# Performance work log

Measured on AMD Instinct MI355X. Metric: run time of the kernel, lower is better.

Reference implementation:

```python
import jax, jax.numpy as jnp
import numpy as np

NUM_CLASSES = 100
CACHE_SIZE = 50
N_PROTOS = NUM_CLASSES * CACHE_SIZE  # 5000
FEAT_DIM = 128
BATCH = 2048
NVIEWS = 2
TEMP = 0.1
EPSILON = 0.05
PROTO_M = 0.99
TOPK = 10
LAMBDA_PCON = 1.0
SINKHORN_ITERS = 3


def _l1norm(x, axis):
    return x / jnp.clip(jnp.sum(jnp.abs(x), axis=axis, keepdims=True), 1e-12)


def _l2norm(x, axis=-1):
    return x / jnp.clip(jnp.linalg.norm(x, axis=axis, keepdims=True), 1e-12)


def _sinkhorn(feats, protos):
    # torch uses out.detach(): Q carries no gradient
    out = jax.lax.stop_gradient(feats @ protos.T)  # [N, K]
    Q = jnp.exp(out / EPSILON).T                   # [K, N]
    K_, B_ = Q.shape
    Q = Q / jnp.sum(Q)
    for _ in range(SINKHORN_ITERS):
        Q = _l1norm(Q, axis=1) / K_   # row L1 normalize
        Q = _l1norm(Q, axis=0) / B_   # col L1 normalize
    return (Q * B_).T                 # [N, K]


def _topk_mask(x, k):
    _, idx = jax.lax.top_k(x, k)
    rows = jnp.arange(x.shape[0])[:, None]
    return jnp.zeros_like(x).at[rows, idx].set(1.0)


def reference(features, targets, beta, protos):
    # features: [B, V, D] -> [V*B, D] (view-major, matches torch.cat(torch.unbind(dim=1)))
    feats = jnp.transpose(features, (1, 0, 2)).reshape(-1, FEAT_DIM)
    labels = jnp.tile(targets, NVIEWS)                              # [N]
    contrast_labels = jnp.tile(jnp.arange(NUM_CLASSES), CACHE_SIZE)  # [K]
    mask = (labels[:, None] == contrast_labels[None, :]).astype(feats.dtype)  # [N, K]

    # ---- mle_loss ----
    Q = _sinkhorn(feats, jax.lax.stop_gradient(protos))
    update_mask = mask * Q
    tkm = _topk_mask(update_mask, TOPK)
    update_mask = _l1norm(tkm * update_mask, axis=1)

    update_features = update_mask.T @ feats                         # [K, D]
    protos_new = PROTO_M * protos + (1.0 - PROTO_M) * update_features
    sim_mean = jax.lax.stop_gradient(
        jnp.mean(jnp.sum(_l2norm(update_features, 1) * _l2norm(protos, 1), axis=1)))
    protos2 = _l2norm(protos_new, axis=1)

    Q2 = _sinkhorn(feats, jax.lax.stop_gradient(protos2))
    logits = jax.nn.softplus(feats @ jax.lax.stop_gradient(protos2).T / TEMP)  # [N, K]

    loss_mask = mask * Q2
    # NOTE: original code top-ks update_mask (already normalized) here, not loss_mask
    tkm2 = _topk_mask(update_mask, TOPK)
    loss_mask = _l1norm(tkm2 * loss_mask, axis=1)
    masked_logits = loss_mask * logits

    positive_logits = mask * logits
    negative_logits = logits * (1.0 - mask)
    imp = jax.lax.stop_gradient(jnp.exp(beta * jnp.log(negative_logits + 1e-10)))
    total_logits = positive_logits + imp * negative_logits

    pos = jnp.sum(masked_logits, axis=1)                             # [N]
    neg = jnp.log(jnp.sum(jnp.exp(total_logits), axis=1, keepdims=True))  # [N, 1]
    # faithful to the torch broadcast: [N] - [N,1] -> [N, N]
    mle = -jnp.mean(pos - neg)

    # ---- proto_contra ----
    pn = _l2norm(protos2, axis=1)                                    # [K, D]
    plabels = jnp.tile(jnp.arange(NUM_CLASSES), CACHE_SIZE)
    pmask = (plabels[:, None] == plabels[None, :]).astype(pn.dtype)
    tau = jax.lax.stop_gradient((1.0 + (0.5 - sim_mean)) * 0.4)
    adc = pn @ pn.T / tau
    lg = adc - jax.lax.stop_gradient(jnp.max(adc, axis=1, keepdims=True))
    lmask = 1.0 - jnp.eye(N_PROTOS, dtype=pn.dtype)
    pmask = pmask * lmask
    ppos = jnp.sum(_l1norm(pmask, axis=1) * lg, axis=1)
    pneg = jnp.log(jnp.sum(lmask * jnp.exp(lg), axis=1))
    pcon = -jnp.mean(ppos - pneg)

    return mle + LAMBDA_PCON * pcon


def setup_inputs() -> dict:
    key = jax.random.key(0)
    k1, k2, k3 = jax.random.split(key, 3)
    features = jax.random.normal(k1, (BATCH, NVIEWS, FEAT_DIM), dtype=jnp.float32)
    features = _l2norm(features, axis=-1)  # unit-norm embeddings keep exp(./eps) finite
    targets = jax.random.randint(k2, (BATCH,), 0, NUM_CLASSES)
    beta = jnp.float32(0.5)
    protos = _l2norm(jax.random.uniform(k3, (N_PROTOS, FEAT_DIM), dtype=jnp.float32), axis=-1)
    return {"features": features, "targets": targets, "beta": beta, "protos": protos}
```

## Files before the change

### kernel.cpp

```cpp
#include <hip/hip_runtime.h>
#include <math.h>

constexpr int NUM_CLASSES = 100;
constexpr int CACHE_SIZE  = 50;
constexpr int NPROT       = 5000;
constexpr int FD          = 128;
constexpr int BATCH       = 2048;
constexpr int NROWS       = 4096;
constexpr int TOPK        = 10;
constexpr float INV_EPS   = 20.0f;
constexpr float INV_TEMP  = 10.0f;
constexpr float PROTO_M   = 0.99f;
constexpr int PLD         = 5120;
constexpr int SROWS       = 16;
constexpr int NSLOT       = NROWS / SROWS;
constexpr int NTILE       = 40;
constexpr int NTRI        = NTILE * (NTILE + 1) / 2;


typedef __attribute__((ext_vector_type(8))) short bf16x8;
typedef __attribute__((ext_vector_type(4))) float f32x4;
typedef __attribute__((ext_vector_type(4))) _Float16 f16x4;
typedef __attribute__((ext_vector_type(8))) _Float16 f16x8;

__device__ __forceinline__ float blockReduceSum(float v) {
  __shared__ float tmp[8];
  const int lane = threadIdx.x & 63;
  const int wid  = threadIdx.x >> 6;
  #pragma unroll
  for (int o = 32; o > 0; o >>= 1) v += __shfl_down(v, o, 64);
  __syncthreads();
  if (lane == 0) tmp[wid] = v;
  __syncthreads();
  const int nw = (blockDim.x + 63) >> 6;
  float s = 0.f;
  for (int i = 0; i < nw; ++i) s += tmp[i];
  return s;
}

__device__ __forceinline__ short f2bf(float x) {
  union { float f; unsigned u; } v; v.f = x;
  const unsigned r = v.u + 0x7fffu + ((v.u >> 16) & 1u);
  return (short)(r >> 16);
}

__global__ void k_build_split(const float* __restrict__ features,
                              const float* __restrict__ protos,
                              float* __restrict__ feats,
                              short* __restrict__ fb, short* __restrict__ pb) {
  constexpr int NF4 = NROWS * (FD / 4);
  constexpr int NP4 = NPROT * FD / 4;
  const int t = blockIdx.x * 256 + threadIdx.x;
  if (t < NF4) {
    const int n  = t >> 5;
    const int d4 = (t & 31) << 2;
    const int b  = n & (BATCH - 1);
    const int v  = n >> 11;
    const float4 src = *reinterpret_cast<const float4*>(features + ((size_t)b * 2 + v) * FD + d4);
    *reinterpret_cast<float4*>(feats + (size_t)n * FD + d4) = src;
    short4 h;
    h.x = f2bf(src.x); h.y = f2bf(src.y); h.z = f2bf(src.z); h.w = f2bf(src.w);
    *reinterpret_cast<short4*>(fb + (size_t)n * FD + d4) = h;
  } else if (t - NF4 < NP4) {
    const int u = t - NF4;
    const float4 v = *reinterpret_cast<const float4*>(protos + (size_t)u * 4);
    short4 h;
    h.x = f2bf(v.x); h.y = f2bf(v.y); h.z = f2bf(v.z); h.w = f2bf(v.w);
    *reinterpret_cast<short4*>(pb + (size_t)u * 4) = h;
  }
}

__global__ __launch_bounds__(256) void k_gemm_mfma(
    const short* __restrict__ A, const short* __restrict__ B,
    int Nb, _Float16* __restrict__ C, float* __restrict__ colpart) {
  __shared__ __align__(16) short Bs[128 * 64];
  __shared__ float red[4][128];
  const int tid  = threadIdx.x;
  const int wid  = tid >> 6;
  const int lane = tid & 63;
  const int lr   = lane & 15;
  const int kg   = lane >> 4;
  const int m0   = blockIdx.y * 128 + wid * 32;
  const int n0   = blockIdx.x * 128;

  f32x4 acc[2][8];
  #pragma unroll
  for (int i = 0; i < 2; ++i)
    #pragma unroll
    for (int j = 0; j < 8; ++j) acc[i][j] = (f32x4){0.f, 0.f, 0.f, 0.f};

  bool cval[8];
  #pragma unroll
  for (int j = 0; j < 8; ++j) cval[j] = (n0 + j * 16 + lr < Nb);

  const int scol = tid >> 1;
  const int sk   = (tid & 1) * 32;
  const int gcol = min(n0 + scol, Nb - 1);

  #pragma unroll
  for (int h = 0; h < 2; ++h) {
    const int k0 = h * 64;
    if (h) __syncthreads();
    #pragma unroll
    for (int u = 0; u < 4; ++u) {
      const int kk2 = sk + u * 8;
      const bf16x8 vb = *reinterpret_cast<const bf16x8*>(B + (size_t)gcol * FD + k0 + kk2);
      const int byteoff = (scol * 128 + kk2 * 2) ^ ((scol & 7) << 4);
      *reinterpret_cast<bf16x8*>(reinterpret_cast<char*>(&Bs[0]) + byteoff) = vb;
    }
    __syncthreads();
    #pragma unroll
    for (int kk = 0; kk < 2; ++kk) {
      const int kb = k0 + kk * 32 + kg * 8;
      bf16x8 av[2], bv[8];
      #pragma unroll
      for (int i = 0; i < 2; ++i)
        av[i] = *reinterpret_cast<const bf16x8*>(A + (size_t)(m0 + i * 16 + lr) * FD + kb);
      #pragma unroll
      for (int j = 0; j < 8; ++j) {
        const int col = j * 16 + lr;
        const int bo = (col * 128 + (kk * 32 + kg * 8) * 2) ^ ((col & 7) << 4);
        bv[j] = *reinterpret_cast<const bf16x8*>(reinterpret_cast<const char*>(&Bs[0]) + bo);
      }
      #pragma unroll
      for (int i = 0; i < 2; ++i)
        #pragma unroll
        for (int j = 0; j < 8; ++j)
          acc[i][j] = __builtin_amdgcn_mfma_f32_16x16x32_bf16(av[i], bv[j], acc[i][j], 0, 0, 0);
    }
  }

  float csum[8];
  #pragma unroll
  for (int j = 0; j < 8; ++j) csum[j] = 0.f;
  #pragma unroll
  for (int i = 0; i < 2; ++i) {
    const int rbase = m0 + i * 16 + kg * 4;
    #pragma unroll
    for (int j = 0; j < 8; ++j) {
      if (!cval[j]) continue;
      const int col = n0 + j * 16 + lr;
      #pragma unroll
      for (int q = 0; q < 4; ++q) {
        const float tval = __expf(acc[i][j][q] * INV_TEMP);
        const _Float16 tf = (_Float16)tval;
        C[(size_t)(rbase + q) * NPROT + col] = tf;
        const float t32 = (float)tf;
        csum[j] = fmaf(t32, t32, csum[j]);
      }
    }
  }
  __syncthreads();
  #pragma unroll
  for (int j = 0; j < 8; ++j) {
    float v = csum[j];
    v += __shfl_xor(v, 16, 64);
    v += __shfl_xor(v, 32, 64);
    if (lane < 16) red[wid][j * 16 + lane] = v;
  }
  __syncthreads();
  if (tid < 128) {
    const int col = n0 + tid;
    if (col < Nb) {
      const float t = red[0][tid] + red[1][tid] + red[2][tid] + red[3][tid];
      colpart[(size_t)blockIdx.y * PLD + col] = t;
    }
  }
}

template <bool WITH_MLE>
__global__ __launch_bounds__(512) void k_sink_fused(const _Float16* __restrict__ big,
                                                    const float* __restrict__ Rin,
                                                    float* __restrict__ part,
                                                    float* __restrict__ semain,
                                                    const float* __restrict__ beta_ptr) {
  __shared__ float Cl[SROWS];
  const int r0   = blockIdx.x * SROWS;
  const int wid  = threadIdx.x >> 6;
  const int lane = threadIdx.x & 63;
  float beta = 0.f;
  bool bhalf = false;
  if constexpr (WITH_MLE) {
    beta = beta_ptr[0];
    bhalf = (beta == 0.5f);
  }
  #pragma unroll
  for (int rr = 0; rr < SROWS / 8; ++rr) {
    const int r = rr * 8 + wid;
    const _Float16* row = big + (size_t)(r0 + r) * NPROT;
    float s = 0.f, se = 0.f;
    for (int idx = lane; idx < NPROT / 8; idx += 64) {
      const f16x8 v = *reinterpret_cast<const f16x8*>(row + idx * 8);
      const float4 q0 = *reinterpret_cast<const float4*>(Rin + idx * 8);
      const float4 q1 = *reinterpret_cast<const float4*>(Rin + idx * 8 + 4);
      float rt[8], rq[8];
      #pragma unroll
      for (int e = 0; e < 8; ++e) rt[e] = (float)v[e];
      rq[0] = q0.x; rq[1] = q0.y; rq[2] = q0.z; rq[3] = q0.w;
      rq[4] = q1.x; rq[5] = q1.y; rq[6] = q1.z; rq[7] = q1.w;
      #pragma unroll
      for (int e = 0; e < 8; ++e)
        s = fmaf(rt[e] * rt[e], rq[e], s);
      if constexpr (WITH_MLE) {
        #pragma unroll
        for (int e = 0; e < 8; ++e) {
          const float l = __logf(1.f + rt[e]);
          const float lb = l + 1e-10f;
          const float imp = bhalf ? sqrtf(lb) : __expf(beta * __logf(lb));
          se += __expf(imp * l);
        }
      }
    }
    #pragma unroll
    for (int o = 32; o > 0; o >>= 1) {
      s += __shfl_down(s, o, 64);
      if constexpr (WITH_MLE) se += __shfl_down(se, o, 64);
    }
    if (lane == 0) {
      Cl[r] = 1.0f / s;
      if constexpr (WITH_MLE) semain[r0 + r] = se;
    }
  }
  __syncthreads();
  for (int k4 = threadIdx.x * 4; k4 < NPROT; k4 += 2048) {
    float s[4] = {0.f, 0.f, 0.f, 0.f};
    #pragma unroll
    for (int r = 0; r < SROWS; ++r) {
      const f16x4 v = *reinterpret_cast<const f16x4*>(big + (size_t)(r0 + r) * NPROT + k4);
      const float c = Cl[r];
      #pragma unroll
      for (int e = 0; e < 4; ++e) {
        const float t = (float)v[e];
        s[e] = fmaf(t * t, c, s[e]);
      }
    }
    *reinterpret_cast<float4*>(part + (size_t)blockIdx.x * PLD + k4) =
        make_float4(s[0], s[1], s[2], s[3]);
  }
}

__global__ __launch_bounds__(512) void k_red_slots(const float* __restrict__ part,
                                                   int nslots, float* __restrict__ R) {
  __shared__ float red[8][64];
  const int g  = threadIdx.x >> 6;
  const int kk = threadIdx.x & 63;
  const int k  = blockIdx.x * 64 + kk;
  float s = 0.f;
  if (k < NPROT) {
    const int per = nslots >> 3;
    const int b0 = g * per, b1 = b0 + per;
    for (int b = b0; b < b1; ++b) s += part[(size_t)b * PLD + k];
  }
  red[g][kk] = s;
  __syncthreads();
  if (threadIdx.x < 64 && k < NPROT) {
    float t = 0.f;
    #pragma unroll
    for (int g2 = 0; g2 < 8; ++g2) t += red[g2][kk];
    R[k] = 1.0f / t;
  }
}

__global__ __launch_bounds__(256) void k_top10(const _Float16* __restrict__ out1,
                                               const float* __restrict__ R3,
                                               const int* __restrict__ targets,
                                               float* __restrict__ wsel) {
  const int n = blockIdx.x * 4 + (threadIdx.x >> 6);
  const int lane = threadIdx.x & 63;
  const int c = targets[n & (BATCH - 1)];
  float cur = -1.0f, orig = -1.0f;
  if (lane < CACHE_SIZE) {
    const int k = c + lane * NUM_CLASSES;
    const float t = (float)out1[(size_t)n * NPROT + k];
    cur = t * t * R3[k];
    orig = cur;
  }
  float tvsum = 0.f;
  bool selme = false;
  #pragma unroll
  for (int i = 0; i < TOPK; ++i) {
    float bv = cur;
    int   bj = lane;
    #pragma unroll
    for (int o = 32; o > 0; o >>= 1) {
      const float ov = __shfl_xor(bv, o, 64);
      const int   oj = __shfl_xor(bj, o, 64);
      if (ov > bv || (ov == bv && oj < bj)) { bv = ov; bj = oj; }
    }
    tvsum += bv;
    if (lane == bj) { cur = -2.0f; selme = true; }
  }
  tvsum = fmaxf(tvsum, 1e-12f);
  if (lane < CACHE_SIZE)
    wsel[(size_t)n * CACHE_SIZE + lane] = selme ? orig / tvsum : 0.f;
}

__global__ __launch_bounds__(1024) void k_prep(const int* __restrict__ targets,
                                               int* __restrict__ classbase,
                                               int* __restrict__ rowlist) {
  __shared__ int t[BATCH];
  __shared__ short chcnt[8][NUM_CLASSES];
  __shared__ int   chpre[8][NUM_CLASSES];
  __shared__ int   ctot[NUM_CLASSES];
  __shared__ int   base[NUM_CLASSES + 1];
  for (int i = threadIdx.x; i < BATCH; i += 1024) t[i] = targets[i];
  __syncthreads();
  if (threadIdx.x < 8 * NUM_CLASSES) {
    const int ch = threadIdx.x / NUM_CLASSES;
    const int c  = threadIdx.x % NUM_CLASSES;
    int m = 0;
    const int i0 = ch << 8;
    for (int i = i0; i < i0 + 256; ++i) m += (t[i] == c);
    chcnt[ch][c] = (short)m;
  }
  __syncthreads();
  if (threadIdx.x < NUM_CLASSES) {
    const int c = threadIdx.x;
    int s = 0;
    #pragma unroll
    for (int ch = 0; ch < 8; ++ch) { chpre[ch][c] = s; s += chcnt[ch][c]; }
    ctot[c] = s;
  }
  __syncthreads();
  if (threadIdx.x == 0) {
    int s = 0;
    for (int c = 0; c < NUM_CLASSES; ++c) { base[c] = s; s += 2 * ctot[c]; }
    base[NUM_CLASSES] = s;
  }
  __syncthreads();
  if (threadIdx.x <= NUM_CLASSES) classbase[threadIdx.x] = base[threadIdx.x];
  for (int b = threadIdx.x; b < BATCH; b += 1024) {
    const int c  = t[b];
    const int ch = b >> 8;
    int r = chpre[ch][c];
    for (int i = ch << 8; i < b; ++i) r += (t[i] == c);
    const int bs  = base[c];
    const int cnt = (base[c + 1] - bs) >> 1;
    rowlist[bs + r] = b;
    rowlist[bs + cnt + r] = BATCH + b;
  }
}

__global__ __launch_bounds__(128) void k_ufpu(const float* __restrict__ feats,
                                              const float* __restrict__ wsel,
                                              const int* __restrict__ rowlist,
                                              const int* __restrict__ classbase,
                                              const float* __restrict__ protos,
                                              short* __restrict__ pnb,
                                              float* __restrict__ simbuf) {
  const int k = blockIdx.x;
  const int d = threadIdx.x;
  const int c = k % NUM_CLASSES;
  const int j = k / NUM_CLASSES;
  const int b0 = classbase[c], b1 = classbase[c + 1];
  float u = 0.f;
  for (int ii = b0; ii < b1; ++ii) {
    const int n = rowlist[ii];
    const float wv = wsel[(size_t)n * CACHE_SIZE + j];
    if (wv != 0.f) u = fmaf(wv, feats[(size_t)n * FD + d], u);
  }
  const float p = protos[(size_t)k * FD + d];
  const float pnew = PROTO_M * p + (1.0f - PROTO_M) * u;
  const float spp = blockReduceSum(p * p);
  const float suu = blockReduceSum(u * u);
  const float sup = blockReduceSum(u * p);
  const float snn = blockReduceSum(pnew * pnew);
  const float x = pnew / fmaxf(sqrtf(snn), 1e-12f);
  pnb[(size_t)k * FD + d] = f2bf(x);
  if (d == 0)
    simbuf[k] = sup / (fmaxf(sqrtf(suu), 1e-12f) * fmaxf(sqrtf(spp), 1e-12f));
}

__global__ void k_tau(const float* __restrict__ simbuf, float* __restrict__ scalars) {
  float s = 0.f;
  for (int k = threadIdx.x; k < NPROT; k += 256) s += simbuf[k];
  s = blockReduceSum(s);
  if (threadIdx.x == 0) {
    const float sim_mean = s / (float)NPROT;
    scalars[0] = (1.0f + (0.5f - sim_mean)) * 0.4f;
  }
}

__global__ __launch_bounds__(256) void k_mle_fin(const _Float16* __restrict__ out2,
                                                 const float* __restrict__ R3,
                                                 const int* __restrict__ targets,
                                                 const float* __restrict__ wsel,
                                                 const float* __restrict__ beta_ptr,
                                                 const float* __restrict__ semain,
                                                 float* __restrict__ rowres) {
  const int n = blockIdx.x * 4 + (threadIdx.x >> 6);
  const int lane = threadIdx.x & 63;
  const int c = targets[n & (BATCH - 1)];
  const float beta = beta_ptr[0];
  const bool bhalf = (beta == 0.5f);
  float corr = 0.f, swl = 0.f, sw = 0.f;
  if (lane < CACHE_SIZE) {
    const int k = c + lane * NUM_CLASSES;
    const float t = (float)out2[(size_t)n * NPROT + k];
    const float l = __logf(1.f + t);
    const float lb = l + 1e-10f;
    const float imp = bhalf ? sqrtf(lb) : __expf(beta * __logf(lb));
    corr = (1.f + t) - __expf(imp * l);
    if (wsel[(size_t)n * CACHE_SIZE + lane] > 0.f) {
      const float w2 = t * t * R3[k];
      swl = w2 * l;
      sw  = w2;
    }
  }
  #pragma unroll
  for (int o = 32; o > 0; o >>= 1) {
    corr += __shfl_down(corr, o, 64);
    swl  += __shfl_down(swl,  o, 64);
    sw   += __shfl_down(sw,   o, 64);
  }
  if (lane == 0)
    rowres[n] = __logf(semain[n] + corr) - swl / fmaxf(sw, 1e-12f);
}

__global__ __launch_bounds__(256) void k_pcon_mfma(
    const short* __restrict__ P, const float* __restrict__ scalars,
    float* __restrict__ part_neg, float* __restrict__ part_pos) {
  __shared__ __align__(16) short Bs[128 * 64];
  int tdec = blockIdx.x, by = 0;
  while (tdec >= NTILE - by) { tdec -= NTILE - by; ++by; }
  const int bx = by + tdec;
  const bool diag = (bx == by);

  const int tid  = threadIdx.x;
  const int wid  = tid >> 6;
  const int lane = tid & 63;
  const int lr   = lane & 15;
  const int kg   = lane >> 4;
  const int k0r  = by * 128 + wid * 32;
  const int l0   = bx * 128;
  const float invtau = 1.0f / scalars[0];

  f32x4 acc[2][8];
  #pragma unroll
  for (int i = 0; i < 2; ++i)
    #pragma unroll
    for (int j = 0; j < 8; ++j) acc[i][j] = (f32x4){0.f, 0.f, 0.f, 0.f};

  int rowa[2];
  #pragma unroll
  for (int i = 0; i < 2; ++i) {
    const int r = k0r + i * 16 + lr;
    rowa[i] = (r < NPROT) ? r : (NPROT - 1);
  }
  bool cval[8];
  #pragma unroll
  for (int j = 0; j < 8; ++j) cval[j] = (l0 + j * 16 + lr < NPROT);

  const int scol = tid >> 1;
  const int sk   = (tid & 1) * 32;
  const int gcol = min(l0 + scol, NPROT - 1);

  #pragma unroll
  for (int h = 0; h < 2; ++h) {
    const int k0 = h * 64;
    if (h) __syncthreads();
    #pragma unroll
    for (int u = 0; u < 4; ++u) {
      const int kk2 = sk + u * 8;
      const bf16x8 vb = *reinterpret_cast<const bf16x8*>(P + (size_t)gcol * FD + k0 + kk2);
      const int byteoff = (scol * 128 + kk2 * 2) ^ ((scol & 7) << 4);
      *reinterpret_cast<bf16x8*>(reinterpret_cast<char*>(&Bs[0]) + byteoff) = vb;
    }
    __syncthreads();
    #pragma unroll
    for (int kk = 0; kk < 2; ++kk) {
      const int kb = k0 + kk * 32 + kg * 8;
      bf16x8 av[2], bv[8];
      #pragma unroll
      for (int i = 0; i < 2; ++i)
        av[i] = *reinterpret_cast<const bf16x8*>(P + (size_t)rowa[i] * FD + kb);
      #pragma unroll
      for (int j = 0; j < 8; ++j) {
        const int col = j * 16 + lr;
        const int bo = (col * 128 + (kk * 32 + kg * 8) * 2) ^ ((col & 7) << 4);
        bv[j] = *reinterpret_cast<const bf16x8*>(reinterpret_cast<const char*>(&Bs[0]) + bo);
      }
      #pragma unroll
      for (int i = 0; i < 2; ++i)
        #pragma unroll
        for (int j = 0; j < 8; ++j)
          acc[i][j] = __builtin_amdgcn_mfma_f32_16x16x32_bf16(av[i], bv[j], acc[i][j], 0, 0, 0);
    }
  }

  int ccls[8];
  #pragma unroll
  for (int j = 0; j < 8; ++j) ccls[j] = (l0 + j * 16 + lr) % NUM_CLASSES;
  float cneg[8], cpos[8];
  #pragma unroll
  for (int j = 0; j < 8; ++j) { cneg[j] = 0.f; cpos[j] = 0.f; }

  #pragma unroll
  for (int i = 0; i < 2; ++i) {
    float sneg[4] = {0.f, 0.f, 0.f, 0.f};
    float spos[4] = {0.f, 0.f, 0.f, 0.f};
    const int rbase = k0r + i * 16 + kg * 4;
    #pragma unroll
    for (int q = 0; q < 4; ++q) {
      const int rg = rbase + q;
      if (rg >= NPROT) continue;
      const int rcls = rg % NUM_CLASSES;
      #pragma unroll
      for (int j = 0; j < 8; ++j) {
        const int cg = l0 + j * 16 + lr;
        if (!cval[j]) continue;
        if (diag && cg == rg) continue;
        const float lg = fmaf(acc[i][j][q], invtau, -invtau);
        const float e  = __expf(lg);
        sneg[q] += e;
        cneg[j] += e;
        if (ccls[j] == rcls) { spos[q] += lg; cpos[j] += lg; }
      }
    }
    #pragma unroll
    for (int q = 0; q < 4; ++q) {
      float sn = sneg[q], sp = spos[q];
      #pragma unroll
      for (int off = 8; off > 0; off >>= 1) {
        sn += __shfl_xor(sn, off, 64);
        sp += __shfl_xor(sp, off, 64);
      }
      if (lr == 0) {
        const int rg = rbase + q;
        if (rg < NPROT) {
          part_neg[(size_t)bx * PLD + rg] = sn;
          part_pos[(size_t)bx * PLD + rg] = sp;
        }
      }
    }
  }

  if (!diag) {
    __syncthreads();
    float* redn = reinterpret_cast<float*>(&Bs[0]);
    float* redp = redn + 512;
    #pragma unroll
    for (int j = 0; j < 8; ++j) {
      float cn = cneg[j];
      cn += __shfl_xor(cn, 16, 64);
      cn += __shfl_xor(cn, 32, 64);
      float cp = cpos[j];
      cp += __shfl_xor(cp, 16, 64);
      cp += __shfl_xor(cp, 32, 64);
      if (lane < 16) {
        redn[wid * 128 + j * 16 + lane] = cn;
        redp[wid * 128 + j * 16 + lane] = cp;
      }
    }
    __syncthreads();
    if (tid < 128) {
      const int cg = l0 + tid;
      if (cg < NPROT) {
        const float tn = redn[tid] + redn[128 + tid] + redn[256 + tid] + redn[384 + tid];
        const float tp = redp[tid] + redp[128 + tid] + redp[256 + tid] + redp[384 + tid];
        part_neg[(size_t)by * PLD + cg] = tn;
        part_pos[(size_t)by * PLD + cg] = tp;
      }
    }
  }
}

__global__ __launch_bounds__(256) void k_pcon_fin(const float* __restrict__ part_neg,
                                                  const float* __restrict__ part_pos,
                                                  float* __restrict__ pconbuf) {
  __shared__ float rn[4][64], rp[4][64];
  const int g  = threadIdx.x >> 6;
  const int kk = threadIdx.x & 63;
  const int k  = blockIdx.x * 64 + kk;
  float sn = 0.f, sp = 0.f;
  if (k < NPROT) {
    for (int b = g * 10; b < g * 10 + 10; ++b) {
      sn += part_neg[(size_t)b * PLD + k];
      sp += part_pos[(size_t)b * PLD + k];
    }
  }
  rn[g][kk] = sn; rp[g][kk] = sp;
  __syncthreads();
  if (threadIdx.x < 64 && k < NPROT) {
    const float tn = rn[0][kk] + rn[1][kk] + rn[2][kk] + rn[3][kk];
    const float tp = rp[0][kk] + rp[1][kk] + rp[2][kk] + rp[3][kk];
    pconbuf[k] = __logf(tn) - tp * (1.0f / (float)(CACHE_SIZE - 1));
  }
}

__global__ void k_final(const float* __restrict__ rowres,
                        const float* __restrict__ pconbuf,
                        float* __restrict__ outp) {
  float s1 = 0.f, s2 = 0.f;
  for (int i = threadIdx.x; i < NROWS; i += 256) s1 += rowres[i];
  for (int i = threadIdx.x; i < NPROT; i += 256) s2 += pconbuf[i];
  s1 = blockReduceSum(s1);
  s2 = blockReduceSum(s2);
  if (threadIdx.x == 0) outp[0] = s1 / (float)NROWS + s2 / (float)NPROT;
}

extern "C" void kernel_launch(void* const* d_in, const int* in_sizes, int n_in,
                              void* d_out, int out_size, void* d_ws, size_t ws_size,
                              hipStream_t stream) {
  (void)in_sizes; (void)n_in; (void)out_size; (void)ws_size;
  const float* features = (const float*)d_in[0];
  const int*   targets  = (const int*)d_in[1];
  const float* beta     = (const float*)d_in[2];
  const float* protos   = (const float*)d_in[3];
  float* outp = (float*)d_out;

  char* basep = (char*)d_ws;
  size_t off = 0;
  auto alloc = [&](size_t bytes) -> void* {
    void* p = basep + off;
    off = (off + bytes + 255) & ~(size_t)255;
    return p;
  };
  _Float16* big  = (_Float16*)alloc((size_t)NROWS * NPROT * 2);
  float* feats   = (float*)alloc((size_t)NROWS * FD * 4);
  short* fb      = (short*)alloc((size_t)NROWS * FD * 2);
  short* pb      = (short*)alloc((size_t)NPROT * FD * 2);
  float* part    = (float*)alloc((size_t)NSLOT * PLD * 4);
  float* Rk      = (float*)alloc(NPROT * 4);
  float* wsel    = (float*)alloc((size_t)NROWS * CACHE_SIZE * 4);
  int*   rowlist = (int*)alloc(NROWS * 4);
  int*   classbase = (int*)alloc((NUM_CLASSES + 1) * 4);
  float* simbuf  = (float*)alloc(NPROT * 4);
  float* scalars = (float*)alloc(64);
  float* semain  = (float*)alloc(NROWS * 4);
  float* rowres  = (float*)alloc(NROWS * 4);
  float* pconbuf = (float*)alloc(NPROT * 4);
  float* pneg    = (float*)alloc((size_t)NTILE * PLD * 4);
  float* ppos    = (float*)alloc((size_t)NTILE * PLD * 4);

  k_build_split<<<1138, 256, 0, stream>>>(features, protos, feats, fb, pb);
  k_prep<<<1, 1024, 0, stream>>>(targets, classbase, rowlist);

  k_gemm_mfma<<<dim3(40, 32), 256, 0, stream>>>(fb, pb, NPROT, big, part);
  k_red_slots<<<79, 512, 0, stream>>>(part, 32, Rk);
  k_sink_fused<false><<<NSLOT, 512, 0, stream>>>(big, Rk, part, nullptr, nullptr);
  k_red_slots<<<79, 512, 0, stream>>>(part, NSLOT, Rk);
  k_sink_fused<false><<<NSLOT, 512, 0, stream>>>(big, Rk, part, nullptr, nullptr);
  k_red_slots<<<79, 512, 0, stream>>>(part, NSLOT, Rk);

  k_top10<<<NROWS / 4, 256, 0, stream>>>(big, Rk, targets, wsel);
  k_ufpu<<<NPROT, 128, 0, stream>>>(feats, wsel, rowlist, classbase, protos, pb, simbuf);
  k_tau<<<1, 256, 0, stream>>>(simbuf, scalars);

  k_gemm_mfma<<<dim3(40, 32), 256, 0, stream>>>(fb, pb, NPROT, big, part);
  k_red_slots<<<79, 512, 0, stream>>>(part, 32, Rk);
  k_sink_fused<false><<<NSLOT, 512, 0, stream>>>(big, Rk, part, nullptr, nullptr);
  k_red_slots<<<79, 512, 0, stream>>>(part, NSLOT, Rk);
  k_sink_fused<true><<<NSLOT, 512, 0, stream>>>(big, Rk, part, semain, beta);
  k_red_slots<<<79, 512, 0, stream>>>(part, NSLOT, Rk);

  k_mle_fin<<<NROWS / 4, 256, 0, stream>>>(big, Rk, targets, wsel, beta, semain, rowres);
  k_pcon_mfma<<<NTRI, 256, 0, stream>>>(pb, scalars, pneg, ppos);
  k_pcon_fin<<<79, 256, 0, stream>>>(pneg, ppos, pconbuf);
  k_final<<<1, 256, 0, stream>>>(rowres, pconbuf, outp);
}
```

Measured before the change: 279.9 us.

## Fuse Sinkhorn passes and slot reductions into one cooperative kernel with grid sync

Replaces the alternating sink_fused / red_slots launches in each Sinkhorn chain with a single cooperative kernel that uses grid.sync() between the column-reduction and row-scaling phases. It also merges the feature/proto conversion kernel with the target bucketing kernel into one launch. The aim is to cut kernel launch overhead and inter-kernel gaps across ten small launches. The risk is grid-sync cost, and it requires all 256 blocks of 512 threads to be co-resident.

```diff
diff --git a/kernel.cpp b/kernel.cpp
--- a/kernel.cpp
+++ b/kernel.cpp
@@ -1,5 +1,8 @@
 #include <hip/hip_runtime.h>
+#include <hip/hip_cooperative_groups.h>
 #include <math.h>
+
+namespace cg = cooperative_groups;
 
 constexpr int NUM_CLASSES = 100;
 constexpr int CACHE_SIZE  = 50;
@@ -8,7 +11,6 @@
 constexpr int BATCH       = 2048;
 constexpr int NROWS       = 4096;
 constexpr int TOPK        = 10;
-constexpr float INV_EPS   = 20.0f;
 constexpr float INV_TEMP  = 10.0f;
 constexpr float PROTO_M   = 0.99f;
 constexpr int PLD         = 5120;
@@ -44,29 +46,74 @@
   return (short)(r >> 16);
 }
 
-__global__ void k_build_split(const float* __restrict__ features,
-                              const float* __restrict__ protos,
-                              float* __restrict__ feats,
-                              short* __restrict__ fb, short* __restrict__ pb) {
+__global__ __launch_bounds__(1024) void k_build_prep(
+    const float* __restrict__ features, const float* __restrict__ protos,
+    const int* __restrict__ targets,
+    float* __restrict__ feats, short* __restrict__ fb, short* __restrict__ pb,
+    int* __restrict__ classbase, int* __restrict__ rowlist) {
   constexpr int NF4 = NROWS * (FD / 4);
   constexpr int NP4 = NPROT * FD / 4;
-  const int t = blockIdx.x * 256 + threadIdx.x;
-  if (t < NF4) {
-    const int n  = t >> 5;
-    const int d4 = (t & 31) << 2;
-    const int b  = n & (BATCH - 1);
-    const int v  = n >> 11;
-    const float4 src = *reinterpret_cast<const float4*>(features + ((size_t)b * 2 + v) * FD + d4);
-    *reinterpret_cast<float4*>(feats + (size_t)n * FD + d4) = src;
-    short4 h;
-    h.x = f2bf(src.x); h.y = f2bf(src.y); h.z = f2bf(src.z); h.w = f2bf(src.w);
-    *reinterpret_cast<short4*>(fb + (size_t)n * FD + d4) = h;
-  } else if (t - NF4 < NP4) {
-    const int u = t - NF4;
-    const float4 v = *reinterpret_cast<const float4*>(protos + (size_t)u * 4);
-    short4 h;
-    h.x = f2bf(v.x); h.y = f2bf(v.y); h.z = f2bf(v.z); h.w = f2bf(v.w);
-    *reinterpret_cast<short4*>(pb + (size_t)u * 4) = h;
+  __shared__ int t[BATCH];
+  __shared__ short chcnt[8][NUM_CLASSES];
+  __shared__ int   chpre[8][NUM_CLASSES];
+  __shared__ int   ctot[NUM_CLASSES];
+  __shared__ int   base[NUM_CLASSES + 1];
+  if (blockIdx.x < 285) {
+    const int w = blockIdx.x * 1024 + threadIdx.x;
+    if (w < NF4) {
+      const int n  = w >> 5;
+      const int d4 = (w & 31) << 2;
+      const int b  = n & (BATCH - 1);
+      const int v  = n >> 11;
+      const float4 src = *reinterpret_cast<const float4*>(features + ((size_t)b * 2 + v) * FD + d4);
+      *reinterpret_cast<float4*>(feats + (size_t)n * FD + d4) = src;
+      short4 h;
+      h.x = f2bf(src.x); h.y = f2bf(src.y); h.z = f2bf(src.z); h.w = f2bf(src.w);
+      *reinterpret_cast<short4*>(fb + (size_t)n * FD + d4) = h;
+    } else if (w - NF4 < NP4) {
+      const int u = w - NF4;
+      const float4 v = *reinterpret_cast<const float4*>(protos + (size_t)u * 4);
+      short4 h;
+      h.x = f2bf(v.x); h.y = f2bf(v.y); h.z = f2bf(v.z); h.w = f2bf(v.w);
+      *reinterpret_cast<short4*>(pb + (size_t)u * 4) = h;
+    }
+    return;
+  }
+  for (int i = threadIdx.x; i < BATCH; i += 1024) t[i] = targets[i];
+  __syncthreads();
+  if (threadIdx.x < 8 * NUM_CLASSES) {
+    const int ch = threadIdx.x / NUM_CLASSES;
+    const int c  = threadIdx.x % NUM_CLASSES;
+    int m = 0;
+    const int i0 = ch << 8;
+    for (int i = i0; i < i0 + 256; ++i) m += (t[i] == c);
+    chcnt[ch][c] = (short)m;
+  }
+  __syncthreads();
+  if (threadIdx.x < NUM_CLASSES) {
+    const int c = threadIdx.x;
+    int s = 0;
+    #pragma unroll
+    for (int ch = 0; ch < 8; ++ch) { chpre[ch][c] = s; s += chcnt[ch][c]; }
+    ctot[c] = s;
+  }
+  __syncthreads();
+  if (threadIdx.x == 0) {
+    int s = 0;
+    for (int c = 0; c < NUM_CLASSES; ++c) { base[c] = s; s += 2 * ctot[c]; }
+    base[NUM_CLASSES] = s;
+  }
+  __syncthreads();
+  if (threadIdx.x <= NUM_CLASSES) classbase[threadIdx.x] = base[threadIdx.x];
+  for (int b = threadIdx.x; b < BATCH; b += 1024) {
+    const int c  = t[b];
+    const int ch = b >> 8;
+    int r = chpre[ch][c];
+    for (int i = ch << 8; i < b; ++i) r += (t[i] == c);
+    const int bs  = base[c];
+    const int cnt = (base[c + 1] - bs) >> 1;
+    rowlist[bs + r] = b;
+    rowlist[bs + cnt + r] = BATCH + b;
   }
 }
 
@@ -169,21 +216,13 @@
 }
 
 template <bool WITH_MLE>
-__global__ __launch_bounds__(512) void k_sink_fused(const _Float16* __restrict__ big,
-                                                    const float* __restrict__ Rin,
-                                                    float* __restrict__ part,
-                                                    float* __restrict__ semain,
-                                                    const float* __restrict__ beta_ptr) {
-  __shared__ float Cl[SROWS];
-  const int r0   = blockIdx.x * SROWS;
-  const int wid  = threadIdx.x >> 6;
-  const int lane = threadIdx.x & 63;
-  float beta = 0.f;
-  bool bhalf = false;
-  if constexpr (WITH_MLE) {
-    beta = beta_ptr[0];
-    bhalf = (beta == 0.5f);
-  }
+__device__ __forceinline__ void sink_pass(const _Float16* __restrict__ big,
+                                          const float* __restrict__ Rin,
+                                          float* __restrict__ part,
+                                          float* __restrict__ semain,
+                                          float beta, bool bhalf,
+                                          int r0, int bid, int wid, int lane,
+                                          int tid, float* Cl) {
   #pragma unroll
   for (int rr = 0; rr < SROWS / 8; ++rr) {
     const int r = rr * 8 + wid;
@@ -222,7 +261,7 @@
     }
   }
   __syncthreads();
-  for (int k4 = threadIdx.x * 4; k4 < NPROT; k4 += 2048) {
+  for (int k4 = tid * 4; k4 < NPROT; k4 += 2048) {
     float s[4] = {0.f, 0.f, 0.f, 0.f};
     #pragma unroll
     for (int r = 0; r < SROWS; ++r) {
@@ -234,31 +273,55 @@
         s[e] = fmaf(t * t, c, s[e]);
       }
     }
-    *reinterpret_cast<float4*>(part + (size_t)blockIdx.x * PLD + k4) =
+    *reinterpret_cast<float4*>(part + (size_t)bid * PLD + k4) =
         make_float4(s[0], s[1], s[2], s[3]);
   }
-}
-
-__global__ __launch_bounds__(512) void k_red_slots(const float* __restrict__ part,
-                                                   int nslots, float* __restrict__ R) {
-  __shared__ float red[8][64];
-  const int g  = threadIdx.x >> 6;
-  const int kk = threadIdx.x & 63;
-  const int k  = blockIdx.x * 64 + kk;
-  float s = 0.f;
-  if (k < NPROT) {
-    const int per = nslots >> 3;
-    const int b0 = g * per, b1 = b0 + per;
-    for (int b = b0; b < b1; ++b) s += part[(size_t)b * PLD + k];
-  }
-  red[g][kk] = s;
-  __syncthreads();
-  if (threadIdx.x < 64 && k < NPROT) {
-    float t = 0.f;
-    #pragma unroll
-    for (int g2 = 0; g2 < 8; ++g2) t += red[g2][kk];
-    R[k] = 1.0f / t;
-  }
+  __syncthreads();
+}
+
+template <bool WITH_MLE>
+__global__ __launch_bounds__(512) void k_sink_chain(
+    const _Float16* __restrict__ big, float* __restrict__ part,
+    float* __restrict__ Rk, float* __restrict__ semain,
+    const float* __restrict__ beta_ptr) {
+  cg::grid_group grid = cg::this_grid();
+  __shared__ float Cl[SROWS];
+  const int bid  = blockIdx.x;
+  const int tid  = threadIdx.x;
+  const int wid  = tid >> 6;
+  const int lane = tid & 63;
+  const int r0   = bid * SROWS;
+  float beta = 0.f;
+  bool bhalf = false;
+  if constexpr (WITH_MLE) {
+    beta = beta_ptr[0];
+    bhalf = (beta == 0.5f);
+  }
+
+  auto reduce_slots = [&](int nslots) {
+    const int w = bid * 512 + tid;
+    const int k = w >> 3;
+    const int g = w & 7;
+    if (k < NPROT) {
+      const int per = nslots >> 3;
+      float s = 0.f;
+      for (int b = g * per; b < (g + 1) * per; ++b) s += part[(size_t)b * PLD + k];
+      s += __shfl_xor(s, 1, 64);
+      s += __shfl_xor(s, 2, 64);
+      s += __shfl_xor(s, 4, 64);
+      if (g == 0) Rk[k] = 1.0f / s;
+    }
+  };
+
+  reduce_slots(32);
+  grid.sync();
+  sink_pass<false>(big, Rk, part, nullptr, 0.f, false, r0, bid, wid, lane, tid, Cl);
+  grid.sync();
+  reduce_slots(NSLOT);
+  grid.sync();
+  sink_pass<WITH_MLE>(big, Rk, part, semain, beta, bhalf, r0, bid, wid, lane, tid, Cl);
+  grid.sync();
+  reduce_slots(NSLOT);
 }
 
 __global__ __launch_bounds__(256) void k_top10(const _Float16* __restrict__ out1,
@@ -293,52 +356,6 @@
   tvsum = fmaxf(tvsum, 1e-12f);
   if (lane < CACHE_SIZE)
     wsel[(size_t)n * CACHE_SIZE + lane] = selme ? orig / tvsum : 0.f;
-}
-
-__global__ __launch_bounds__(1024) void k_prep(const int* __restrict__ targets,
-                                               int* __restrict__ classbase,
-                                               int* __restrict__ rowlist) {
-  __shared__ int t[BATCH];
-  __shared__ short chcnt[8][NUM_CLASSES];
-  __shared__ int   chpre[8][NUM_CLASSES];
-  __shared__ int   ctot[NUM_CLASSES];
-  __shared__ int   base[NUM_CLASSES + 1];
-  for (int i = threadIdx.x; i < BATCH; i += 1024) t[i] = targets[i];
-  __syncthreads();
-  if (threadIdx.x < 8 * NUM_CLASSES) {
-    const int ch = threadIdx.x / NUM_CLASSES;
-    const int c  = threadIdx.x % NUM_CLASSES;
-    int m = 0;
-    const int i0 = ch << 8;
-    for (int i = i0; i < i0 + 256; ++i) m += (t[i] == c);
-    chcnt[ch][c] = (short)m;
-  }
-  __syncthreads();
-  if (threadIdx.x < NUM_CLASSES) {
-    const int c = threadIdx.x;
-    int s = 0;
-    #pragma unroll
-    for (int ch = 0; ch < 8; ++ch) { chpre[ch][c] = s; s += chcnt[ch][c]; }
-    ctot[c] = s;
-  }
-  __syncthreads();
-  if (threadIdx.x == 0) {
-    int s = 0;
-    for (int c = 0; c < NUM_CLASSES; ++c) { base[c] = s; s += 2 * ctot[c]; }
-    base[NUM_CLASSES] = s;
-  }
-  __syncthreads();
-  if (threadIdx.x <= NUM_CLASSES) classbase[threadIdx.x] = base[threadIdx.x];
-  for (int b = threadIdx.x; b < BATCH; b += 1024) {
-    const int c  = t[b];
-    const int ch = b >> 8;
-    int r = chpre[ch][c];
-    for (int i = ch << 8; i < b; ++i) r += (t[i] == c);
-    const int bs  = base[c];
-    const int cnt = (base[c + 1] - bs) >> 1;
-    rowlist[bs + r] = b;
-    rowlist[bs + cnt + r] = BATCH + b;
-  }
 }
 
 __global__ __launch_bounds__(128) void k_ufpu(const float* __restrict__ feats,
@@ -633,26 +650,27 @@
   float* pneg    = (float*)alloc((size_t)NTILE * PLD * 4);
   float* ppos    = (float*)alloc((size_t)NTILE * PLD * 4);
 
-  k_build_split<<<1138, 256, 0, stream>>>(features, protos, feats, fb, pb);
-  k_prep<<<1, 1024, 0, stream>>>(targets, classbase, rowlist);
+  k_build_prep<<<286, 1024, 0, stream>>>(features, protos, targets,
+                                         feats, fb, pb, classbase, rowlist);
+
+  void* chain_args[5];
+  chain_args[0] = (void*)&big;
+  chain_args[1] = (void*)&part;
+  chain_args[2] = (void*)&Rk;
+  chain_args[3] = (void*)&semain;
+  chain_args[4] = (void*)&beta;
 
   k_gemm_mfma<<<dim3(40, 32), 256, 0, stream>>>(fb, pb, NPROT, big, part);
-  k_red_slots<<<79, 512, 0, stream>>>(part, 32, Rk);
-  k_sink_fused<false><<<NSLOT, 512, 0, stream>>>(big, Rk, part, nullptr, nullptr);
-  k_red_slots<<<79, 512, 0, stream>>>(part, NSLOT, Rk);
-  k_sink_fused<false><<<NSLOT, 512, 0, stream>>>(big, Rk, part, nullptr, nullptr);
-  k_red_slots<<<79, 512, 0, stream>>>(part, NSLOT, Rk);
+  hipLaunchCooperativeKernel(reinterpret_cast<void*>(&k_sink_chain<false>),
+                             dim3(NSLOT), dim3(512), chain_args, 0, stream);
 
   k_top10<<<NROWS / 4, 256, 0, stream>>>(big, Rk, targets, wsel);
   k_ufpu<<<NPROT, 128, 0, stream>>>(feats, wsel, rowlist, classbase, protos, pb, simbuf);
   k_tau<<<1, 256, 0, stream>>>(simbuf, scalars);
 
   k_gemm_mfma<<<dim3(40, 32), 256, 0, stream>>>(fb, pb, NPROT, big, part);
-  k_red_slots<<<79, 512, 0, stream>>>(part, 32, Rk);
-  k_sink_fused<false><<<NSLOT, 512, 0, stream>>>(big, Rk, part, nullptr, nullptr);
-  k_red_slots<<<79, 512, 0, stream>>>(part, NSLOT, Rk);
-  k_sink_fused<true><<<NSLOT, 512, 0, stream>>>(big, Rk, part, semain, beta);
-  k_red_slots<<<79, 512, 0, stream>>>(part, NSLOT, Rk);
+  hipLaunchCooperativeKernel(reinterpret_cast<void*>(&k_sink_chain<true>),
+                             dim3(NSLOT), dim3(512), chain_args, 0, stream);
 
   k_mle_fin<<<NROWS / 4, 256, 0, stream>>>(big, Rk, targets, wsel, beta, semain, rowres);
   k_pcon_mfma<<<NTRI, 256, 0, stream>>>(pb, scalars, pneg, ppos);
```

After: 492.1 us. 1.76x slower.
